# Kernel optimization log

Measured on AMD Instinct MI355X. Metric: run time of the kernel, lower is better.

The kernel has to match this reference:

```python
import jax, jax.numpy as jnp
import numpy as np
import math

DIM = 1024
SEQ = 2048
BATCH = 4
LN_EPS = 1e-5


def _linear_params(key, fan_in, fan_out):
    # torch nn.Linear default init: U(-1/sqrt(fan_in), 1/sqrt(fan_in))
    k1, k2 = jax.random.split(key)
    bound = 1.0 / math.sqrt(fan_in)
    W = jax.random.uniform(k1, (fan_out, fan_in), minval=-bound, maxval=bound, dtype=jnp.float32)
    b = jax.random.uniform(k2, (fan_out,), minval=-bound, maxval=bound, dtype=jnp.float32)
    return W, b


def setup_inputs() -> dict:
    key = jax.random.key(0)
    ks = jax.random.split(key, 9)
    x = jax.random.normal(ks[0], (BATCH, SEQ, DIM), dtype=jnp.float32)
    base_phases = jax.random.normal(ks[1], (SEQ, DIM), dtype=jnp.float32) * math.pi
    Wk, bk = _linear_params(ks[2], DIM, DIM)
    Wv, bv = _linear_params(ks[3], DIM, DIM)
    Wq, bq = _linear_params(ks[4], DIM, DIM)
    Wkm, bkm = _linear_params(ks[5], DIM, DIM)
    Wqm, bqm = _linear_params(ks[6], DIM, DIM)
    Wo, bo = _linear_params(ks[7], DIM, DIM)
    mod_scale = jnp.ones((1,), dtype=jnp.float32) * 0.1
    ln_g = jnp.ones((DIM,), dtype=jnp.float32)
    ln_b = jnp.zeros((DIM,), dtype=jnp.float32)
    return dict(x=x, base_phases=base_phases, Wk=Wk, bk=bk, Wv=Wv, bv=bv,
                Wq=Wq, bq=bq, Wkm=Wkm, bkm=bkm, Wqm=Wqm, bqm=bqm,
                mod_scale=mod_scale, ln_g=ln_g, ln_b=ln_b, Wo=Wo, bo=bo)


def _lin(x, W, b):
    return jnp.einsum('bsd,ed->bse', x, W) + b


def reference(x, base_phases, Wk, bk, Wv, bv, Wq, bq, Wkm, bkm, Wqm, bqm,
              mod_scale, ln_g, ln_b, Wo, bo):
    dim = x.shape[-1]
    base_phase = base_phases[None, :, :]  # [1, S, D]
    key = _lin(x, Wk, bk)
    value = _lin(x, Wv, bv)
    query = _lin(x, Wq, bq)
    key_phase = base_phase + _lin(key, Wkm, bkm) * mod_scale
    query_phase = base_phase + _lin(query, Wqm, bqm) * mod_scale
    # bind value with complex phasor exp(i*key_phase), prefix-sum over seq
    mem_real = jnp.cumsum(value * jnp.cos(key_phase), axis=1)
    mem_imag = jnp.cumsum(value * jnp.sin(key_phase), axis=1)
    # phase-matched retrieval: Re(mem * exp(-i*query_phase))
    retrieved = (mem_real * jnp.cos(query_phase) + mem_imag * jnp.sin(query_phase))
    retrieved = retrieved / math.sqrt(dim)
    # LayerNorm then output projection
    mu = jnp.mean(retrieved, axis=-1, keepdims=True)
    var = jnp.var(retrieved, axis=-1, keepdims=True)
    normed = (retrieved - mu) * jax.lax.rsqrt(var + LN_EPS) * ln_g + ln_b
    out = _lin(normed, Wo, bo)
    return x + out
```

## Files before the change

### kernel.cpp

```cpp
#include <hip/hip_runtime.h>
#include <math.h>

#define DIM 1024
#define SEQ 2048
#define BATCH 4
#define ROWS (BATCH*SEQ)
#define CHUNKS 128
#define CLEN (SEQ/CHUNKS)
#define N3 3072
#define LN_EPS 1e-5f
#define NTK 16

typedef unsigned short ushort_t;
typedef __attribute__((ext_vector_type(8))) short bf16x8;
typedef __attribute__((ext_vector_type(4))) float f32x4;

static const size_t NE = (size_t)ROWS * DIM;
static const size_t WN = (size_t)DIM * DIM;

__device__ inline ushort_t f2bf(float f) {
    union { float f; unsigned u; } v; v.f = f;
    unsigned r = v.u + 0x7FFFu + ((v.u >> 16) & 1u);
    return (ushort_t)(r >> 16);
}
__device__ inline float bf2f(ushort_t u) { return __uint_as_float((unsigned)u << 16); }

__global__ __launch_bounds__(256)
void prep_all_k(const float* __restrict__ x,   const float* __restrict__ Wv,
                const float* __restrict__ Wo,  const float* __restrict__ Wkm,
                const float* __restrict__ Wqm, const float* __restrict__ Wk,
                const float* __restrict__ Wq,  const float* __restrict__ bk,
                const float* __restrict__ bkm, const float* __restrict__ bq,
                const float* __restrict__ bqm,
                ushort_t* __restrict__ xbf,   ushort_t* __restrict__ W3,
                ushort_t* __restrict__ wo_b,  ushort_t* __restrict__ wkm_b,
                ushort_t* __restrict__ wqm_b, ushort_t* __restrict__ wkT,
                ushort_t* __restrict__ wqT,
                float* __restrict__ bck, float* __restrict__ bcq)
{
    const int blk = blockIdx.x;
    const int t = threadIdx.x;
    __shared__ ushort_t tile[32][33];

    if (blk < 6144) {
        size_t e = ((size_t)blk * 256 + t) * 8;
        const float* src; ushort_t* dst; size_t off;
        if      (e < NE)          { src = x;   dst = xbf;   off = e; }
        else if (e < NE + WN)     { src = Wv;  dst = W3;    off = e - NE; }
        else if (e < NE + 2*WN)   { src = Wo;  dst = wo_b;  off = e - NE - WN; }
        else if (e < NE + 3*WN)   { src = Wkm; dst = wkm_b; off = e - NE - 2*WN; }
        else                      { src = Wqm; dst = wqm_b; off = e - NE - 3*WN; }
        float4 a = *(const float4*)(src + off);
        float4 b = *(const float4*)(src + off + 4);
        ushort4 lo, hi;
        lo.x = f2bf(a.x); lo.y = f2bf(a.y); lo.z = f2bf(a.z); lo.w = f2bf(a.w);
        hi.x = f2bf(b.x); hi.y = f2bf(b.y); hi.z = f2bf(b.z); hi.w = f2bf(b.w);
        *(ushort4*)(dst + off) = lo;
        *(ushort4*)(dst + off + 4) = hi;
    } else if (blk < 8192) {
        int tb = blk - 6144;
        const float* in = (tb >> 10) ? Wq : Wk;
        ushort_t* out   = (tb >> 10) ? wqT : wkT;
        int tid = tb & 1023;
        int bx = tid & 31, by = tid >> 5;
        int tx = t & 31, ty = t >> 5;
        #pragma unroll
        for (int j = 0; j < 4; ++j) {
            int r = by * 32 + ty + j * 8;
            tile[ty + j * 8][tx] = f2bf(in[(size_t)r * DIM + bx * 32 + tx]);
        }
        __syncthreads();
        #pragma unroll
        for (int j = 0; j < 4; ++j) {
            int r = bx * 32 + ty + j * 8;
            out[(size_t)r * DIM + by * 32 + tx] = tile[tx][ty + j * 8];
        }
    } else {
        int mb = blk - 8192;
        int z = mb >> 8;
        const float* Wm  = z ? Wqm : Wkm;
        const float* bi  = z ? bq  : bk;
        const float* bo_ = z ? bqm : bkm;
        float* bc        = z ? bcq : bck;
        int e = (mb & 255) * 4 + (t >> 6);
        int l = t & 63;
        float s = 0.f;
        #pragma unroll
        for (int j = 0; j < DIM / 64; ++j)
            s += Wm[(size_t)e * DIM + l + j * 64] * bi[l + j * 64];
        #pragma unroll
        for (int o = 32; o >= 1; o >>= 1) s += __shfl_down(s, o);
        if (l == 0) bc[e] = s + bo_[e];
    }
}

__global__ __launch_bounds__(256)
void gemm_combine2(const ushort_t* __restrict__ A0, const ushort_t* __restrict__ W0,
                   ushort_t* __restrict__ C0,
                   const ushort_t* __restrict__ A1, const ushort_t* __restrict__ W1,
                   ushort_t* __restrict__ C1)
{
    const ushort_t* A = blockIdx.z ? A1 : A0;
    const ushort_t* W = blockIdx.z ? W1 : W0;
    ushort_t*       C = blockIdx.z ? C1 : C0;
    __shared__ ushort_t As[128 * 32];
    __shared__ ushort_t Bs[128 * 32];
    const int bm = blockIdx.x * 128;
    const int bn = blockIdx.y * 128;
    const int t = threadIdx.x;
    const int lane = t & 63;
    const int w = t >> 6, wr = w >> 1, wc = w & 1;
    f32x4 acc[4][4] = {};
    const int fr = lane & 15;
    const int kc = (lane >> 4) * 8;
    for (int k0 = 0; k0 < DIM; k0 += 32) {
        #pragma unroll
        for (int i = 0; i < 2; ++i) {
            int c = t + i * 256;
            int row = c >> 2;
            int col = (c & 3) * 8;
            const ushort_t* ga = A + (size_t)(bm + row) * DIM + k0 + col;
            __builtin_amdgcn_global_load_lds(
                (const __attribute__((address_space(1))) void*)ga,
                (__attribute__((address_space(3))) void*)(As + (size_t)c * 8), 16, 0, 0);
            const ushort_t* gb = W + (size_t)(bn + row) * DIM + k0 + col;
            __builtin_amdgcn_global_load_lds(
                (const __attribute__((address_space(1))) void*)gb,
                (__attribute__((address_space(3))) void*)(Bs + (size_t)c * 8), 16, 0, 0);
        }
        __syncthreads();
        bf16x8 af[4], bw[4];
        #pragma unroll
        for (int m2 = 0; m2 < 4; ++m2)
            af[m2] = *(const bf16x8*)(As + (wr * 64 + m2 * 16 + fr) * 32 + kc);
        #pragma unroll
        for (int n2 = 0; n2 < 4; ++n2)
            bw[n2] = *(const bf16x8*)(Bs + (wc * 64 + n2 * 16 + fr) * 32 + kc);
        #pragma unroll
        for (int m2 = 0; m2 < 4; ++m2)
            #pragma unroll
            for (int n2 = 0; n2 < 4; ++n2)
                acc[m2][n2] = __builtin_amdgcn_mfma_f32_16x16x32_bf16(
                    af[m2], bw[n2], acc[m2][n2], 0, 0, 0);
        __syncthreads();
    }
    const int fc = lane & 15;
    const int r0 = (lane >> 4) * 4;
    #pragma unroll
    for (int m2 = 0; m2 < 4; ++m2)
        #pragma unroll
        for (int n2 = 0; n2 < 4; ++n2) {
            int col = bn + wc * 64 + n2 * 16 + fc;
            #pragma unroll
            for (int r = 0; r < 4; ++r) {
                int row = bm + wr * 64 + m2 * 16 + r0 + r;
                C[(size_t)row * DIM + col] = f2bf(acc[m2][n2][r]);
            }
        }
}

template<int MODE, int BN>
__global__ __launch_bounds__(512)
void gemm_pipe(const ushort_t* __restrict__ A, const ushort_t* __restrict__ W,
               const float* __restrict__ bias, const ushort_t* __restrict__ resid,
               void* __restrict__ Cout, int N)
{
    constexpr int NF   = BN / 64;
    constexpr int BUFU = 16384 + BN * 64;
    __shared__ __align__(16) ushort_t lds[2 * BUFU];

    const int bm = blockIdx.x * 256;
    const int bn = blockIdx.y * BN;
    const int t = threadIdx.x;
    const int lane = t & 63;
    const int w = t >> 6;
    const int wr = w >> 2;
    const int wc = w & 3;
    const int fr = lane & 15;
    const int hi = lane >> 4;

    f32x4 acc[8][NF] = {};

    auto SA = [&](int kt, ushort_t* buf, int h) {
        #pragma unroll
        for (int i = 0; i < 2; ++i) {
            int c = t + i * 512;
            int row = c >> 2, sl = c & 3, sg = sl ^ ((row >> 1) & 3);
            const ushort_t* g = A + (size_t)(bm + row) * 1024 + kt * 64 + h * 32 + sg * 8;
            __builtin_amdgcn_global_load_lds(
                (const __attribute__((address_space(1))) void*)g,
                (__attribute__((address_space(3))) void*)(buf + h * 8192 + (size_t)c * 8),
                16, 0, 0);
        }
    };
    auto SBfull = [&](int kt, ushort_t* buf) {
        #pragma unroll
        for (int i = 0; i < 3; ++i) {
            int c = t + i * 512;
            int row = c >> 3, sl = c & 7, sg = sl ^ (row & 7);
            const ushort_t* g = W + (size_t)(bn + row) * 1024 + kt * 64 + sg * 8;
            __builtin_amdgcn_global_load_lds(
                (const __attribute__((address_space(1))) void*)g,
                (__attribute__((address_space(3))) void*)(buf + 16384 + (size_t)c * 8),
                16, 0, 0);
        }
    };
    auto SBh = [&](int kt, ushort_t* buf, int h) {
        int c = t;
        int row = c >> 2, sl = c & 3, sg = sl ^ ((row >> 1) & 3);
        const ushort_t* g = W + (size_t)(bn + row) * 1024 + kt * 64 + h * 32 + sg * 8;
        __builtin_amdgcn_global_load_lds(
            (const __attribute__((address_space(1))) void*)g,
            (__attribute__((address_space(3))) void*)(buf + 16384 + h * (BN * 32) + (size_t)c * 8),
            16, 0, 0);
    };

#define GPHASE(KK, MH, STAGE_STMT)                                           \
    {                                                                        \
        bf16x8 af[4];                                                        \
        _Pragma("unroll")                                                    \
        for (int j = 0; j < 4; ++j) {                                        \
            int row = wr * 128 + ((MH) * 4 + j) * 16 + fr;                   \
            af[j] = *(const bf16x8*)(As + (KK) * 8192 + row * 32 +           \
                                     ((hi ^ ((row >> 1) & 3))) * 8);         \
        }                                                                    \
        if ((MH) == 0) {                                                     \
            _Pragma("unroll")                                                \
            for (int nf = 0; nf < NF; ++nf) {                                \
                int row = wc * (BN / 4) + nf * 16 + fr;                      \
                if (BN == 192)                                               \
                    bw[nf] = *(const bf16x8*)(Bs + row * 64 +                \
                                 (((KK) * 4 + hi) ^ (row & 7)) * 8);         \
                else                                                         \
                    bw[nf] = *(const bf16x8*)(Bs + (KK) * (BN * 32) + row * 32 + \
                                 ((hi ^ ((row >> 1) & 3))) * 8);             \
            }                                                                \
        }                                                                    \
        STAGE_STMT;                                                          \
        __builtin_amdgcn_s_barrier();                                        \
        asm volatile("s_waitcnt lgkmcnt(0)" ::: "memory");                   \
        __builtin_amdgcn_sched_barrier(0);                                   \
        __builtin_amdgcn_s_setprio(1);                                       \
        _Pragma("unroll")                                                    \
        for (int j = 0; j < 4; ++j)                                          \
            _Pragma("unroll")                                                \
            for (int nf = 0; nf < NF; ++nf)                                  \
                acc[(MH) * 4 + j][nf] = __builtin_amdgcn_mfma_f32_16x16x32_bf16( \
                    af[j], bw[nf], acc[(MH) * 4 + j][nf], 0, 0, 0);          \
        __builtin_amdgcn_s_setprio(0);                                       \
        __builtin_amdgcn_s_barrier();                                        \
    }

    if constexpr (BN == 192) {
        SBfull(0, lds); SA(0, lds, 0); SA(0, lds, 1);
    } else {
        SA(0, lds, 0); SBh(0, lds, 0); SA(0, lds, 1); SBh(0, lds, 1);
    }

    for (int tt = 0; tt < NTK; ++tt) {
        ushort_t* base = lds + (tt & 1) * BUFU;
        ushort_t* nbuf = lds + ((tt + 1) & 1) * BUFU;
        const ushort_t* As = base;
        const ushort_t* Bs = base + 16384;
        const bool st = (tt + 1 < NTK);
        bf16x8 bw[NF];

        if constexpr (BN == 192) asm volatile("s_waitcnt vmcnt(2)" ::: "memory");
        else                     asm volatile("s_waitcnt vmcnt(3)" ::: "memory");
        __builtin_amdgcn_s_barrier();

        if constexpr (BN == 192) {
            GPHASE(0, 0, if (st) SBfull(tt + 1, nbuf));
            GPHASE(0, 1, if (st) SA(tt + 1, nbuf, 0));
        } else {
            GPHASE(0, 0, if (st) SA(tt + 1, nbuf, 0));
            GPHASE(0, 1, if (st) SBh(tt + 1, nbuf, 0));
        }

        if (st) {
            if constexpr (BN == 192) asm volatile("s_waitcnt vmcnt(5)" ::: "memory");
            else                     asm volatile("s_waitcnt vmcnt(3)" ::: "memory");
        } else {
            asm volatile("s_waitcnt vmcnt(0)" ::: "memory");
        }
        __builtin_amdgcn_s_barrier();

        if constexpr (BN == 192) {
            GPHASE(1, 0, if (st) SA(tt + 1, nbuf, 1));
            GPHASE(1, 1, );
        } else {
            GPHASE(1, 0, if (st) SA(tt + 1, nbuf, 1));
            GPHASE(1, 1, if (st) SBh(tt + 1, nbuf, 1));
        }
    }
#undef GPHASE

    const int fc = fr;
    const int r0 = hi * 4;
    #pragma unroll
    for (int m2 = 0; m2 < 8; ++m2)
        #pragma unroll
        for (int n2 = 0; n2 < NF; ++n2) {
            int col = bn + wc * (BN / 4) + n2 * 16 + fc;
            float bv;
            if (MODE == 6) bv = (col < 1024) ? bias[col] : 0.0f;
            else           bv = bias[col];
            #pragma unroll
            for (int r = 0; r < 4; ++r) {
                int row = bm + wr * 128 + m2 * 16 + r0 + r;
                size_t idx = (size_t)row * N + col;
                float v = acc[m2][n2][r] + bv;
                if (MODE == 4) ((float*)Cout)[idx] = v + bf2f(resid[idx]);
                else           ((ushort_t*)Cout)[idx] = f2bf(v);
            }
        }
}

__global__ __launch_bounds__(256)
void phase_scan1_k(const ushort_t* __restrict__ act3, const float* __restrict__ bp,
                   const float* __restrict__ bck, const float* __restrict__ ms_p,
                   float* __restrict__ sumr, float* __restrict__ sumi)
{
    const int blk = blockIdx.x;
    const int b = blk >> 7;
    const int c = blk & (CHUNKS - 1);
    const int d0 = threadIdx.x * 4;
    const float ms = ms_p[0];
    const float4 bc4 = *(const float4*)(bck + d0);
    float sr0 = 0.f, sr1 = 0.f, sr2 = 0.f, sr3 = 0.f;
    float si0 = 0.f, si1 = 0.f, si2 = 0.f, si3 = 0.f;
    const size_t row0 = (size_t)b * SEQ + (size_t)c * CLEN;

    #pragma unroll 2
    for (int s = 0; s < CLEN; ++s) {
        size_t row = row0 + s;
        ushort4 v4 = *(const ushort4*)(act3 + row * N3 + d0);
        ushort4 k4 = *(const ushort4*)(act3 + row * N3 + 1024 + d0);
        float4 bp4 = *(const float4*)(bp + ((size_t)(c * CLEN + s)) * DIM + d0);
        float vv, kp, sn, cs;
        vv = bf2f(v4.x); kp = bp4.x + (bf2f(k4.x) + bc4.x) * ms;
        __sincosf(kp, &sn, &cs); sr0 += vv * cs; si0 += vv * sn;
        vv = bf2f(v4.y); kp = bp4.y + (bf2f(k4.y) + bc4.y) * ms;
        __sincosf(kp, &sn, &cs); sr1 += vv * cs; si1 += vv * sn;
        vv = bf2f(v4.z); kp = bp4.z + (bf2f(k4.z) + bc4.z) * ms;
        __sincosf(kp, &sn, &cs); sr2 += vv * cs; si2 += vv * sn;
        vv = bf2f(v4.w); kp = bp4.w + (bf2f(k4.w) + bc4.w) * ms;
        __sincosf(kp, &sn, &cs); sr3 += vv * cs; si3 += vv * sn;
    }
    int sgid = (b * CHUNKS + c) * DIM + d0;
    *(float4*)(sumr + sgid) = make_float4(sr0, sr1, sr2, sr3);
    *(float4*)(sumi + sgid) = make_float4(si0, si1, si2, si3);
}

__global__ __launch_bounds__(256)
void scan_pass2(float* __restrict__ sumr, float* __restrict__ sumi)
{
    int wid  = (blockIdx.x * 256 + threadIdx.x) >> 6;
    int lane = threadIdx.x & 63;
    int b = wid >> 10;
    int d = wid & (DIM - 1);
    int i0 = (b * CHUNKS + 2 * lane) * DIM + d;
    int i1 = i0 + DIM;
    float r0 = sumr[i0], r1 = sumr[i1];
    float s0 = sumi[i0], s1 = sumi[i1];
    float pr = r0 + r1, pi = s0 + s1;
    float er = pr, ei = pi;
    #pragma unroll
    for (int o = 1; o < 64; o <<= 1) {
        float tr = __shfl_up(er, o);
        float ti = __shfl_up(ei, o);
        if (lane >= o) { er += tr; ei += ti; }
    }
    er -= pr; ei -= pi;
    sumr[i0] = er;       sumi[i0] = ei;
    sumr[i1] = er + r0;  sumi[i1] = ei + s0;
}

__global__ __launch_bounds__(256)
void scan3_ln_k(const ushort_t* __restrict__ act3, const float* __restrict__ bp,
                const float* __restrict__ bck, const float* __restrict__ bcq,
                const float* __restrict__ ms_p,
                const float* __restrict__ sumr, const float* __restrict__ sumi,
                const float* __restrict__ g, const float* __restrict__ beta,
                ushort_t* __restrict__ normbf)
{
    const int blk = blockIdx.x;
    const int b = blk >> 7;
    const int c = blk & (CHUNKS - 1);
    const int t = threadIdx.x;
    const int d0 = t * 4;
    const float ms = ms_p[0];
    const float4 bk4 = *(const float4*)(bck + d0);
    const float4 bq4 = *(const float4*)(bcq + d0);
    const float inv_sqrt_dim = 0.03125f;

    int sgid = (b * CHUNKS + c) * DIM + d0;
    float4 rrv = *(const float4*)(sumr + sgid);
    float4 riv = *(const float4*)(sumi + sgid);
    float rr0 = rrv.x, rr1 = rrv.y, rr2 = rrv.z, rr3 = rrv.w;
    float ri0 = riv.x, ri1 = riv.y, ri2 = riv.z, ri3 = riv.w;

    const size_t row0 = (size_t)b * SEQ + (size_t)c * CLEN;
    __shared__ float red[CLEN][8];
    const int wv = t >> 6, lane = t & 63;

    float retr[CLEN][4];

    ushort4 v4 = *(const ushort4*)(act3 + row0 * N3 + d0);
    ushort4 k4 = *(const ushort4*)(act3 + row0 * N3 + 1024 + d0);
    ushort4 q4 = *(const ushort4*)(act3 + row0 * N3 + 2048 + d0);
    float4  bp4 = *(const float4*)(bp + (size_t)(c * CLEN) * DIM + d0);

    #pragma unroll
    for (int s = 0; s < CLEN; ++s) {
        ushort4 vc = v4, kc4 = k4, qc = q4; float4 bpc = bp4;
        if (s + 1 < CLEN) {
            size_t row = row0 + s + 1;
            v4  = *(const ushort4*)(act3 + row * N3 + d0);
            k4  = *(const ushort4*)(act3 + row * N3 + 1024 + d0);
            q4  = *(const ushort4*)(act3 + row * N3 + 2048 + d0);
            bp4 = *(const float4*)(bp + (size_t)(c * CLEN + s + 1) * DIM + d0);
        }
        float vv, kp, qp, sk, ck, sq, cq;
        vv = bf2f(vc.x); kp = bpc.x + (bf2f(kc4.x) + bk4.x) * ms;
        __sincosf(kp, &sk, &ck); rr0 += vv * ck; ri0 += vv * sk;
        qp = bpc.x + (bf2f(qc.x) + bq4.x) * ms; __sincosf(qp, &sq, &cq);
        retr[s][0] = (rr0 * cq + ri0 * sq) * inv_sqrt_dim;
        vv = bf2f(vc.y); kp = bpc.y + (bf2f(kc4.y) + bk4.y) * ms;
        __sincosf(kp, &sk, &ck); rr1 += vv * ck; ri1 += vv * sk;
        qp = bpc.y + (bf2f(qc.y) + bq4.y) * ms; __sincosf(qp, &sq, &cq);
        retr[s][1] = (rr1 * cq + ri1 * sq) * inv_sqrt_dim;
        vv = bf2f(vc.z); kp = bpc.z + (bf2f(kc4.z) + bk4.z) * ms;
        __sincosf(kp, &sk, &ck); rr2 += vv * ck; ri2 += vv * sk;
        qp = bpc.z + (bf2f(qc.z) + bq4.z) * ms; __sincosf(qp, &sq, &cq);
        retr[s][2] = (rr2 * cq + ri2 * sq) * inv_sqrt_dim;
        vv = bf2f(vc.w); kp = bpc.w + (bf2f(kc4.w) + bk4.w) * ms;
        __sincosf(kp, &sk, &ck); rr3 += vv * ck; ri3 += vv * sk;
        qp = bpc.w + (bf2f(qc.w) + bq4.w) * ms; __sincosf(qp, &sq, &cq);
        retr[s][3] = (rr3 * cq + ri3 * sq) * inv_sqrt_dim;

        float ssum = retr[s][0] + retr[s][1] + retr[s][2] + retr[s][3];
        float ssq  = retr[s][0]*retr[s][0] + retr[s][1]*retr[s][1]
                   + retr[s][2]*retr[s][2] + retr[s][3]*retr[s][3];
        #pragma unroll
        for (int o = 32; o >= 1; o >>= 1) {
            ssum += __shfl_down(ssum, o);
            ssq  += __shfl_down(ssq, o);
        }
        if (lane == 0) { red[s][wv] = ssum; red[s][wv + 4] = ssq; }
    }

    __syncthreads();

    const float4 gv  = *(const float4*)(g + d0);
    const float4 btv = *(const float4*)(beta + d0);
    #pragma unroll
    for (int s = 0; s < CLEN; ++s) {
        float S  = ((red[s][0] + red[s][1]) + red[s][2]) + red[s][3];
        float SS = ((red[s][4] + red[s][5]) + red[s][6]) + red[s][7];
        float mu  = S * (1.0f / DIM);
        float var = SS * (1.0f / DIM) - mu * mu;
        float rstd = rsqrtf(var + LN_EPS);
        ushort4 o;
        o.x = f2bf((retr[s][0] - mu) * rstd * gv.x + btv.x);
        o.y = f2bf((retr[s][1] - mu) * rstd * gv.y + btv.y);
        o.z = f2bf((retr[s][2] - mu) * rstd * gv.z + btv.z);
        o.w = f2bf((retr[s][3] - mu) * rstd * gv.w + btv.w);
        *(ushort4*)(normbf + (row0 + s) * DIM + d0) = o;
    }
}

extern "C" void kernel_launch(void* const* d_in, const int* in_sizes, int n_in,
                              void* d_out, int out_size, void* d_ws, size_t ws_size,
                              hipStream_t stream)
{
    const float* x   = (const float*)d_in[0];
    const float* bp  = (const float*)d_in[1];
    const float* Wk  = (const float*)d_in[2];
    const float* bk  = (const float*)d_in[3];
    const float* Wv  = (const float*)d_in[4];
    const float* bv  = (const float*)d_in[5];
    const float* Wq  = (const float*)d_in[6];
    const float* bq  = (const float*)d_in[7];
    const float* Wkm = (const float*)d_in[8];
    const float* bkm = (const float*)d_in[9];
    const float* Wqm = (const float*)d_in[10];
    const float* bqm = (const float*)d_in[11];
    const float* ms  = (const float*)d_in[12];
    const float* lng = (const float*)d_in[13];
    const float* lnb = (const float*)d_in[14];
    const float* Wo  = (const float*)d_in[15];
    const float* bo  = (const float*)d_in[16];
    float* out = (float*)d_out;

    ushort_t* act3   = (ushort_t*)d_ws;
    ushort_t* xbf    = act3 + (size_t)ROWS * N3;
    ushort_t* normbf = xbf + NE;
    ushort_t* W3     = normbf + NE;
    ushort_t* wo_b   = W3 + (size_t)N3 * DIM;
    ushort_t* wkm_b  = wo_b + WN;
    ushort_t* wqm_b  = wkm_b + WN;
    ushort_t* wkT_b  = wqm_b + WN;
    ushort_t* wqT_b  = wkT_b + WN;
    float* bck       = (float*)(wqT_b + WN);
    float* bcq       = bck + DIM;
    float* sumr      = bcq + DIM;
    float* sumi      = sumr + (size_t)BATCH * CHUNKS * DIM;

    prep_all_k<<<8704, 256, 0, stream>>>(x, Wv, Wo, Wkm, Wqm, Wk, Wq,
                                         bk, bkm, bq, bqm,
                                         xbf, W3, wo_b, wkm_b, wqm_b,
                                         wkT_b, wqT_b, bck, bcq);

    dim3 gw(DIM / 128, DIM / 128, 2);
    gemm_combine2<<<gw, 256, 0, stream>>>(wkm_b, wkT_b, W3 + WN,
                                          wqm_b, wqT_b, W3 + 2 * WN);

    dim3 g3(32, N3 / 192);
    gemm_pipe<6, 192><<<g3, 512, 0, stream>>>(xbf, W3, bv, nullptr, act3, N3);

    phase_scan1_k<<<BATCH * CHUNKS, 256, 0, stream>>>(act3, bp, bck, ms,
                                                      sumr, sumi);
    scan_pass2<<<(BATCH * DIM) / 4, 256, 0, stream>>>(sumr, sumi);
    scan3_ln_k<<<BATCH * CHUNKS, 256, 0, stream>>>(act3, bp, bck, bcq, ms,
                                                   sumr, sumi, lng, lnb, normbf);

    dim3 gg(32, DIM / 128);
    gemm_pipe<4, 128><<<gg, 512, 0, stream>>>(normbf, wo_b, bo, xbf, out, DIM);
}
```

Baseline: 163.3 us.

## Fuse three scan kernels into one cooperative kernel with grid syncs

Merges the chunk-sum, cross-chunk prefix scan, and retrieval+LayerNorm kernels into a single cooperative launch of 512 blocks, using grid-wide syncs between phases. This removes two kernel launch boundaries and their drain and refill gaps. In exchange it adds two grid barriers. Register pressure also rises, because all phases now share one kernel and the retr array must fit alongside the first phase's state, which can lower occupancy.

```diff
diff --git a/kernel.cpp b/kernel.cpp
--- a/kernel.cpp
+++ b/kernel.cpp
@@ -1,4 +1,5 @@
 #include <hip/hip_runtime.h>
+#include <hip/hip_cooperative_groups.h>
 #include <math.h>
 
 #define DIM 1024
@@ -317,70 +318,10 @@
 }
 
 __global__ __launch_bounds__(256)
-void phase_scan1_k(const ushort_t* __restrict__ act3, const float* __restrict__ bp,
-                   const float* __restrict__ bck, const float* __restrict__ ms_p,
-                   float* __restrict__ sumr, float* __restrict__ sumi)
-{
-    const int blk = blockIdx.x;
-    const int b = blk >> 7;
-    const int c = blk & (CHUNKS - 1);
-    const int d0 = threadIdx.x * 4;
-    const float ms = ms_p[0];
-    const float4 bc4 = *(const float4*)(bck + d0);
-    float sr0 = 0.f, sr1 = 0.f, sr2 = 0.f, sr3 = 0.f;
-    float si0 = 0.f, si1 = 0.f, si2 = 0.f, si3 = 0.f;
-    const size_t row0 = (size_t)b * SEQ + (size_t)c * CLEN;
-
-    #pragma unroll 2
-    for (int s = 0; s < CLEN; ++s) {
-        size_t row = row0 + s;
-        ushort4 v4 = *(const ushort4*)(act3 + row * N3 + d0);
-        ushort4 k4 = *(const ushort4*)(act3 + row * N3 + 1024 + d0);
-        float4 bp4 = *(const float4*)(bp + ((size_t)(c * CLEN + s)) * DIM + d0);
-        float vv, kp, sn, cs;
-        vv = bf2f(v4.x); kp = bp4.x + (bf2f(k4.x) + bc4.x) * ms;
-        __sincosf(kp, &sn, &cs); sr0 += vv * cs; si0 += vv * sn;
-        vv = bf2f(v4.y); kp = bp4.y + (bf2f(k4.y) + bc4.y) * ms;
-        __sincosf(kp, &sn, &cs); sr1 += vv * cs; si1 += vv * sn;
-        vv = bf2f(v4.z); kp = bp4.z + (bf2f(k4.z) + bc4.z) * ms;
-        __sincosf(kp, &sn, &cs); sr2 += vv * cs; si2 += vv * sn;
-        vv = bf2f(v4.w); kp = bp4.w + (bf2f(k4.w) + bc4.w) * ms;
-        __sincosf(kp, &sn, &cs); sr3 += vv * cs; si3 += vv * sn;
-    }
-    int sgid = (b * CHUNKS + c) * DIM + d0;
-    *(float4*)(sumr + sgid) = make_float4(sr0, sr1, sr2, sr3);
-    *(float4*)(sumi + sgid) = make_float4(si0, si1, si2, si3);
-}
-
-__global__ __launch_bounds__(256)
-void scan_pass2(float* __restrict__ sumr, float* __restrict__ sumi)
-{
-    int wid  = (blockIdx.x * 256 + threadIdx.x) >> 6;
-    int lane = threadIdx.x & 63;
-    int b = wid >> 10;
-    int d = wid & (DIM - 1);
-    int i0 = (b * CHUNKS + 2 * lane) * DIM + d;
-    int i1 = i0 + DIM;
-    float r0 = sumr[i0], r1 = sumr[i1];
-    float s0 = sumi[i0], s1 = sumi[i1];
-    float pr = r0 + r1, pi = s0 + s1;
-    float er = pr, ei = pi;
-    #pragma unroll
-    for (int o = 1; o < 64; o <<= 1) {
-        float tr = __shfl_up(er, o);
-        float ti = __shfl_up(ei, o);
-        if (lane >= o) { er += tr; ei += ti; }
-    }
-    er -= pr; ei -= pi;
-    sumr[i0] = er;       sumi[i0] = ei;
-    sumr[i1] = er + r0;  sumi[i1] = ei + s0;
-}
-
-__global__ __launch_bounds__(256)
-void scan3_ln_k(const ushort_t* __restrict__ act3, const float* __restrict__ bp,
+void scan_all_k(const ushort_t* __restrict__ act3, const float* __restrict__ bp,
                 const float* __restrict__ bck, const float* __restrict__ bcq,
                 const float* __restrict__ ms_p,
-                const float* __restrict__ sumr, const float* __restrict__ sumi,
+                float* __restrict__ sumr, float* __restrict__ sumi,
                 const float* __restrict__ g, const float* __restrict__ beta,
                 ushort_t* __restrict__ normbf)
 {
@@ -391,82 +332,137 @@
     const int d0 = t * 4;
     const float ms = ms_p[0];
     const float4 bk4 = *(const float4*)(bck + d0);
-    const float4 bq4 = *(const float4*)(bcq + d0);
-    const float inv_sqrt_dim = 0.03125f;
-
-    int sgid = (b * CHUNKS + c) * DIM + d0;
-    float4 rrv = *(const float4*)(sumr + sgid);
-    float4 riv = *(const float4*)(sumi + sgid);
-    float rr0 = rrv.x, rr1 = rrv.y, rr2 = rrv.z, rr3 = rrv.w;
-    float ri0 = riv.x, ri1 = riv.y, ri2 = riv.z, ri3 = riv.w;
-
     const size_t row0 = (size_t)b * SEQ + (size_t)c * CLEN;
-    __shared__ float red[CLEN][8];
     const int wv = t >> 6, lane = t & 63;
 
-    float retr[CLEN][4];
-
-    ushort4 v4 = *(const ushort4*)(act3 + row0 * N3 + d0);
-    ushort4 k4 = *(const ushort4*)(act3 + row0 * N3 + 1024 + d0);
-    ushort4 q4 = *(const ushort4*)(act3 + row0 * N3 + 2048 + d0);
-    float4  bp4 = *(const float4*)(bp + (size_t)(c * CLEN) * DIM + d0);
-
-    #pragma unroll
-    for (int s = 0; s < CLEN; ++s) {
-        ushort4 vc = v4, kc4 = k4, qc = q4; float4 bpc = bp4;
-        if (s + 1 < CLEN) {
-            size_t row = row0 + s + 1;
-            v4  = *(const ushort4*)(act3 + row * N3 + d0);
-            k4  = *(const ushort4*)(act3 + row * N3 + 1024 + d0);
-            q4  = *(const ushort4*)(act3 + row * N3 + 2048 + d0);
-            bp4 = *(const float4*)(bp + (size_t)(c * CLEN + s + 1) * DIM + d0);
-        }
-        float vv, kp, qp, sk, ck, sq, cq;
-        vv = bf2f(vc.x); kp = bpc.x + (bf2f(kc4.x) + bk4.x) * ms;
-        __sincosf(kp, &sk, &ck); rr0 += vv * ck; ri0 += vv * sk;
-        qp = bpc.x + (bf2f(qc.x) + bq4.x) * ms; __sincosf(qp, &sq, &cq);
-        retr[s][0] = (rr0 * cq + ri0 * sq) * inv_sqrt_dim;
-        vv = bf2f(vc.y); kp = bpc.y + (bf2f(kc4.y) + bk4.y) * ms;
-        __sincosf(kp, &sk, &ck); rr1 += vv * ck; ri1 += vv * sk;
-        qp = bpc.y + (bf2f(qc.y) + bq4.y) * ms; __sincosf(qp, &sq, &cq);
-        retr[s][1] = (rr1 * cq + ri1 * sq) * inv_sqrt_dim;
-        vv = bf2f(vc.z); kp = bpc.z + (bf2f(kc4.z) + bk4.z) * ms;
-        __sincosf(kp, &sk, &ck); rr2 += vv * ck; ri2 += vv * sk;
-        qp = bpc.z + (bf2f(qc.z) + bq4.z) * ms; __sincosf(qp, &sq, &cq);
-        retr[s][2] = (rr2 * cq + ri2 * sq) * inv_sqrt_dim;
-        vv = bf2f(vc.w); kp = bpc.w + (bf2f(kc4.w) + bk4.w) * ms;
-        __sincosf(kp, &sk, &ck); rr3 += vv * ck; ri3 += vv * sk;
-        qp = bpc.w + (bf2f(qc.w) + bq4.w) * ms; __sincosf(qp, &sq, &cq);
-        retr[s][3] = (rr3 * cq + ri3 * sq) * inv_sqrt_dim;
-
-        float ssum = retr[s][0] + retr[s][1] + retr[s][2] + retr[s][3];
-        float ssq  = retr[s][0]*retr[s][0] + retr[s][1]*retr[s][1]
-                   + retr[s][2]*retr[s][2] + retr[s][3]*retr[s][3];
-        #pragma unroll
-        for (int o = 32; o >= 1; o >>= 1) {
-            ssum += __shfl_down(ssum, o);
-            ssq  += __shfl_down(ssq, o);
-        }
-        if (lane == 0) { red[s][wv] = ssum; red[s][wv + 4] = ssq; }
-    }
-
-    __syncthreads();
-
-    const float4 gv  = *(const float4*)(g + d0);
-    const float4 btv = *(const float4*)(beta + d0);
-    #pragma unroll
-    for (int s = 0; s < CLEN; ++s) {
-        float S  = ((red[s][0] + red[s][1]) + red[s][2]) + red[s][3];
-        float SS = ((red[s][4] + red[s][5]) + red[s][6]) + red[s][7];
-        float mu  = S * (1.0f / DIM);
-        float var = SS * (1.0f / DIM) - mu * mu;
-        float rstd = rsqrtf(var + LN_EPS);
-        ushort4 o;
-        o.x = f2bf((retr[s][0] - mu) * rstd * gv.x + btv.x);
-        o.y = f2bf((retr[s][1] - mu) * rstd * gv.y + btv.y);
-        o.z = f2bf((retr[s][2] - mu) * rstd * gv.z + btv.z);
-        o.w = f2bf((retr[s][3] - mu) * rstd * gv.w + btv.w);
-        *(ushort4*)(normbf + (row0 + s) * DIM + d0) = o;
+    {
+        const float4 bc4 = bk4;
+        float sr0 = 0.f, sr1 = 0.f, sr2 = 0.f, sr3 = 0.f;
+        float si0 = 0.f, si1 = 0.f, si2 = 0.f, si3 = 0.f;
+        #pragma unroll 2
+        for (int s = 0; s < CLEN; ++s) {
+            size_t row = row0 + s;
+            ushort4 v4 = *(const ushort4*)(act3 + row * N3 + d0);
+            ushort4 k4 = *(const ushort4*)(act3 + row * N3 + 1024 + d0);
+            float4 bp4 = *(const float4*)(bp + ((size_t)(c * CLEN + s)) * DIM + d0);
+            float vv, kp, sn, cs;
+            vv = bf2f(v4.x); kp = bp4.x + (bf2f(k4.x) + bc4.x) * ms;
+            __sincosf(kp, &sn, &cs); sr0 += vv * cs; si0 += vv * sn;
+            vv = bf2f(v4.y); kp = bp4.y + (bf2f(k4.y) + bc4.y) * ms;
+            __sincosf(kp, &sn, &cs); sr1 += vv * cs; si1 += vv * sn;
+            vv = bf2f(v4.z); kp = bp4.z + (bf2f(k4.z) + bc4.z) * ms;
+            __sincosf(kp, &sn, &cs); sr2 += vv * cs; si2 += vv * sn;
+            vv = bf2f(v4.w); kp = bp4.w + (bf2f(k4.w) + bc4.w) * ms;
+            __sincosf(kp, &sn, &cs); sr3 += vv * cs; si3 += vv * sn;
+        }
+        int sgid = (b * CHUNKS + c) * DIM + d0;
+        *(float4*)(sumr + sgid) = make_float4(sr0, sr1, sr2, sr3);
+        *(float4*)(sumi + sgid) = make_float4(si0, si1, si2, si3);
+    }
+
+    cooperative_groups::this_grid().sync();
+
+    {
+        int wgid = blk * 4 + wv;
+        #pragma unroll
+        for (int j = 0; j < 2; ++j) {
+            int job = wgid + j * 2048;
+            int jb = job >> 10;
+            int jd = job & (DIM - 1);
+            int i0 = (jb * CHUNKS + 2 * lane) * DIM + jd;
+            int i1 = i0 + DIM;
+            float r0 = sumr[i0], r1 = sumr[i1];
+            float s0 = sumi[i0], s1 = sumi[i1];
+            float pr = r0 + r1, pi = s0 + s1;
+            float er = pr, ei = pi;
+            #pragma unroll
+            for (int o = 1; o < 64; o <<= 1) {
+                float tr = __shfl_up(er, o);
+                float ti = __shfl_up(ei, o);
+                if (lane >= o) { er += tr; ei += ti; }
+            }
+            er -= pr; ei -= pi;
+            sumr[i0] = er;       sumi[i0] = ei;
+            sumr[i1] = er + r0;  sumi[i1] = ei + s0;
+        }
+    }
+
+    cooperative_groups::this_grid().sync();
+
+    {
+        const float4 bq4 = *(const float4*)(bcq + d0);
+        const float inv_sqrt_dim = 0.03125f;
+        int sgid = (b * CHUNKS + c) * DIM + d0;
+        float4 rrv = *(const float4*)(sumr + sgid);
+        float4 riv = *(const float4*)(sumi + sgid);
+        float rr0 = rrv.x, rr1 = rrv.y, rr2 = rrv.z, rr3 = rrv.w;
+        float ri0 = riv.x, ri1 = riv.y, ri2 = riv.z, ri3 = riv.w;
+
+        __shared__ float red[CLEN][8];
+        float retr[CLEN][4];
+
+        ushort4 v4 = *(const ushort4*)(act3 + row0 * N3 + d0);
+        ushort4 k4 = *(const ushort4*)(act3 + row0 * N3 + 1024 + d0);
+        ushort4 q4 = *(const ushort4*)(act3 + row0 * N3 + 2048 + d0);
+        float4  bp4 = *(const float4*)(bp + (size_t)(c * CLEN) * DIM + d0);
+
+        #pragma unroll
+        for (int s = 0; s < CLEN; ++s) {
+            ushort4 vc = v4, kc4 = k4, qc = q4; float4 bpc = bp4;
+            if (s + 1 < CLEN) {
+                size_t row = row0 + s + 1;
+                v4  = *(const ushort4*)(act3 + row * N3 + d0);
+                k4  = *(const ushort4*)(act3 + row * N3 + 1024 + d0);
+                q4  = *(const ushort4*)(act3 + row * N3 + 2048 + d0);
+                bp4 = *(const float4*)(bp + (size_t)(c * CLEN + s + 1) * DIM + d0);
+            }
+            float vv, kp, qp, sk, ck, sq, cq;
+            vv = bf2f(vc.x); kp = bpc.x + (bf2f(kc4.x) + bk4.x) * ms;
+            __sincosf(kp, &sk, &ck); rr0 += vv * ck; ri0 += vv * sk;
+            qp = bpc.x + (bf2f(qc.x) + bq4.x) * ms; __sincosf(qp, &sq, &cq);
+            retr[s][0] = (rr0 * cq + ri0 * sq) * inv_sqrt_dim;
+            vv = bf2f(vc.y); kp = bpc.y + (bf2f(kc4.y) + bk4.y) * ms;
+            __sincosf(kp, &sk, &ck); rr1 += vv * ck; ri1 += vv * sk;
+            qp = bpc.y + (bf2f(qc.y) + bq4.y) * ms; __sincosf(qp, &sq, &cq);
+            retr[s][1] = (rr1 * cq + ri1 * sq) * inv_sqrt_dim;
+            vv = bf2f(vc.z); kp = bpc.z + (bf2f(kc4.z) + bk4.z) * ms;
+            __sincosf(kp, &sk, &ck); rr2 += vv * ck; ri2 += vv * sk;
+            qp = bpc.z + (bf2f(qc.z) + bq4.z) * ms; __sincosf(qp, &sq, &cq);
+            retr[s][2] = (rr2 * cq + ri2 * sq) * inv_sqrt_dim;
+            vv = bf2f(vc.w); kp = bpc.w + (bf2f(kc4.w) + bk4.w) * ms;
+            __sincosf(kp, &sk, &ck); rr3 += vv * ck; ri3 += vv * sk;
+            qp = bpc.w + (bf2f(qc.w) + bq4.w) * ms; __sincosf(qp, &sq, &cq);
+            retr[s][3] = (rr3 * cq + ri3 * sq) * inv_sqrt_dim;
+
+            float ssum = retr[s][0] + retr[s][1] + retr[s][2] + retr[s][3];
+            float ssq  = retr[s][0]*retr[s][0] + retr[s][1]*retr[s][1]
+                       + retr[s][2]*retr[s][2] + retr[s][3]*retr[s][3];
+            #pragma unroll
+            for (int o = 32; o >= 1; o >>= 1) {
+                ssum += __shfl_down(ssum, o);
+                ssq  += __shfl_down(ssq, o);
+            }
+            if (lane == 0) { red[s][wv] = ssum; red[s][wv + 4] = ssq; }
+        }
+
+        __syncthreads();
+
+        const float4 gv  = *(const float4*)(g + d0);
+        const float4 btv = *(const float4*)(beta + d0);
+        #pragma unroll
+        for (int s = 0; s < CLEN; ++s) {
+            float S  = ((red[s][0] + red[s][1]) + red[s][2]) + red[s][3];
+            float SS = ((red[s][4] + red[s][5]) + red[s][6]) + red[s][7];
+            float mu  = S * (1.0f / DIM);
+            float var = SS * (1.0f / DIM) - mu * mu;
+            float rstd = rsqrtf(var + LN_EPS);
+            ushort4 o;
+            o.x = f2bf((retr[s][0] - mu) * rstd * gv.x + btv.x);
+            o.y = f2bf((retr[s][1] - mu) * rstd * gv.y + btv.y);
+            o.z = f2bf((retr[s][2] - mu) * rstd * gv.z + btv.z);
+            o.w = f2bf((retr[s][3] - mu) * rstd * gv.w + btv.w);
+            *(ushort4*)(normbf + (row0 + s) * DIM + d0) = o;
+        }
     }
 }
 
@@ -519,11 +515,13 @@
     dim3 g3(32, N3 / 192);
     gemm_pipe<6, 192><<<g3, 512, 0, stream>>>(xbf, W3, bv, nullptr, act3, N3);
 
-    phase_scan1_k<<<BATCH * CHUNKS, 256, 0, stream>>>(act3, bp, bck, ms,
-                                                      sumr, sumi);
-    scan_pass2<<<(BATCH * DIM) / 4, 256, 0, stream>>>(sumr, sumi);
-    scan3_ln_k<<<BATCH * CHUNKS, 256, 0, stream>>>(act3, bp, bck, bcq, ms,
-                                                   sumr, sumi, lng, lnb, normbf);
+    {
+        void* args[] = { (void*)&act3, (void*)&bp, (void*)&bck, (void*)&bcq,
+                         (void*)&ms, (void*)&sumr, (void*)&sumi,
+                         (void*)&lng, (void*)&lnb, (void*)&normbf };
+        hipLaunchCooperativeKernel((void*)scan_all_k, dim3(BATCH * CHUNKS),
+                                   dim3(256), args, 0, stream);
+    }
 
     dim3 gg(32, DIM / 128);
     gemm_pipe<4, 128><<<gg, 512, 0, stream>>>(normbf, wo_b, bo, xbf, out, DIM);
```

Result: slower. 289.0 us (+77.0%).
